# Optimization experiments

Measured on AMD Instinct MI355X. Metric: run time of the kernel, lower is better.

Reference implementation:

```python
import jax, jax.numpy as jnp
import numpy as np

EPS = 1e-5

def setup_inputs() -> dict:
    key = jax.random.key(0)
    kx, kq, kp = jax.random.split(key, 3)
    B, T, d = 4, 4096, 512
    x = jax.random.normal(kx, (B, T, d), dtype=jnp.float32)
    mask = jnp.tril(jnp.ones((T, T), dtype=jnp.int32))  # causal 0/1 mask
    gamma = jnp.ones((d,), dtype=jnp.float32)
    beta = jnp.zeros((d,), dtype=jnp.float32)
    Wqkv = jax.random.normal(kq, (d, 3 * d), dtype=jnp.float32) / np.sqrt(d)
    Wproj = jax.random.normal(kp, (d, d), dtype=jnp.float32) / np.sqrt(d)
    return {"x": x, "mask": mask, "gamma": gamma, "beta": beta, "Wqkv": Wqkv, "Wproj": Wproj}

def reference(x, mask, gamma, beta, Wqkv, Wproj):
    B, T, C = x.shape
    # LayerNorm over last dim
    mu = jnp.mean(x, axis=-1, keepdims=True)
    var = jnp.mean(jnp.square(x - mu), axis=-1, keepdims=True)
    xn = (x - mu) * jax.lax.rsqrt(var + EPS) * gamma + beta
    # QKV projection (no bias)
    qkv = xn @ Wqkv  # [B,T,3C]
    q, k, v = jnp.split(qkv, 3, axis=-1)
    scale = 1.0 / np.sqrt(C)
    dist = jnp.einsum('btc,bsc->bts', q, k) * scale  # [B,T,T]
    dist = jnp.where(mask[:T, :T] == 0, -jnp.inf, dist)
    attn = jax.nn.softmax(dist, axis=-1)
    out = jnp.einsum('bts,bsc->btc', attn, v)
    return out @ Wproj
```

## Files before the change

kernel.cpp:

```cpp
#include <hip/hip_runtime.h>

typedef short bf16x8 __attribute__((ext_vector_type(8)));
typedef float f32x4 __attribute__((ext_vector_type(4)));

#define AS1 __attribute__((address_space(1)))
#define AS3 __attribute__((address_space(3)))

__device__ __forceinline__ void async16(const void* g, void* l) {
    __builtin_amdgcn_global_load_lds((AS1 unsigned*)(unsigned long long)g,
                                     (AS3 unsigned*)l, 16, 0, 0);
}

__device__ __forceinline__ unsigned short f2bf(float f) {
    unsigned u = __builtin_bit_cast(unsigned, f);
    u += 0x7fffu + ((u >> 16) & 1u);
    return (unsigned short)(u >> 16);
}
__device__ __forceinline__ float bf2f(unsigned short s) {
    unsigned u = ((unsigned)s) << 16;
    return __builtin_bit_cast(float, u);
}

__global__ __launch_bounds__(256) void ln_bf16_kernel(
    const float* __restrict__ x, const float* __restrict__ gamma,
    const float* __restrict__ beta, unsigned short* __restrict__ xn, int nrows)
{
    int row = blockIdx.x * 4 + (threadIdx.x >> 6);
    int lane = threadIdx.x & 63;
    if (row >= nrows) return;
    const float4* xr = (const float4*)(x + (size_t)row * 512);
    float4 a = xr[lane], b = xr[lane + 64];
    float s = a.x + a.y + a.z + a.w + b.x + b.y + b.z + b.w;
    #pragma unroll
    for (int m = 1; m < 64; m <<= 1) s += __shfl_xor(s, m);
    float mu = s * (1.0f / 512.0f);
    float dx[8] = {a.x - mu, a.y - mu, a.z - mu, a.w - mu,
                   b.x - mu, b.y - mu, b.z - mu, b.w - mu};
    float ss = 0.f;
    #pragma unroll
    for (int i = 0; i < 8; ++i) ss += dx[i] * dx[i];
    #pragma unroll
    for (int m = 1; m < 64; m <<= 1) ss += __shfl_xor(ss, m);
    float rstd = rsqrtf(ss * (1.0f / 512.0f) + 1e-5f);
    const float4* gp = (const float4*)gamma;
    const float4* bp = (const float4*)beta;
    float4 g0 = gp[lane], g1 = gp[lane + 64], b0 = bp[lane], b1 = bp[lane + 64];
    float y[8];
    y[0] = dx[0] * rstd * g0.x + b0.x; y[1] = dx[1] * rstd * g0.y + b0.y;
    y[2] = dx[2] * rstd * g0.z + b0.z; y[3] = dx[3] * rstd * g0.w + b0.w;
    y[4] = dx[4] * rstd * g1.x + b1.x; y[5] = dx[5] * rstd * g1.y + b1.y;
    y[6] = dx[6] * rstd * g1.z + b1.z; y[7] = dx[7] * rstd * g1.w + b1.w;
    ushort4* orow = (ushort4*)(xn + (size_t)row * 512);
    orow[lane]      = make_ushort4(f2bf(y[0]), f2bf(y[1]), f2bf(y[2]), f2bf(y[3]));
    orow[lane + 64] = make_ushort4(f2bf(y[4]), f2bf(y[5]), f2bf(y[6]), f2bf(y[7]));
}

__global__ __launch_bounds__(256) void transpose_w(
    const float* __restrict__ in, unsigned short* __restrict__ outT, int R, int Cd)
{
    __shared__ float tile[64][65];
    int r0 = blockIdx.x * 64, c0 = blockIdx.y * 64;
    int lr = threadIdx.x >> 6, lc = threadIdx.x & 63;
    #pragma unroll
    for (int i = 0; i < 16; ++i) {
        int r = i * 4 + lr;
        tile[r][lc] = in[(size_t)(r0 + r) * Cd + c0 + lc];
    }
    __syncthreads();
    #pragma unroll
    for (int i = 0; i < 16; ++i) {
        int r = i * 4 + lr;
        outT[(size_t)(c0 + r) * R + r0 + lc] = f2bf(tile[lc][r]);
    }
}

__global__ __launch_bounds__(256) void gemm_qkv(
    const unsigned short* __restrict__ A, const unsigned short* __restrict__ Bt,
    unsigned short* __restrict__ qkOut, unsigned short* __restrict__ vtp)
{
    __shared__ unsigned short As[128 * 64];
    __shared__ unsigned short Bs[128 * 64];
    const int tid = threadIdx.x;
    const int w = tid >> 6, lane = tid & 63, quad = lane >> 4, l15 = lane & 15;
    const int wm = w >> 1, wn = w & 1;
    const size_t m0 = (size_t)blockIdx.x * 128, n0 = (size_t)blockIdx.y * 128;
    f32x4 zero = {0.f, 0.f, 0.f, 0.f};
    f32x4 acc[4][4];
    #pragma unroll
    for (int i = 0; i < 4; ++i)
        #pragma unroll
        for (int j = 0; j < 4; ++j) acc[i][j] = zero;

    for (int k0 = 0; k0 < 512; k0 += 64) {
        __syncthreads();
        #pragma unroll
        for (int r = 0; r < 4; ++r) {
            int s = r * 256 + w * 64 + lane;
            int row = s >> 3, x = s & 7, g = x ^ (row & 7);
            async16(A + (m0 + row) * 512 + k0 + g * 8,
                    (char*)As + (size_t)(r * 256 + w * 64) * 16);
        }
        #pragma unroll
        for (int r = 0; r < 4; ++r) {
            int s = r * 256 + w * 64 + lane;
            int row = s >> 3, x = s & 7, g = x ^ (row & 7);
            async16(Bt + (n0 + row) * 512 + k0 + g * 8,
                    (char*)Bs + (size_t)(r * 256 + w * 64) * 16);
        }
        __syncthreads();
        #pragma unroll
        for (int ks = 0; ks < 2; ++ks) {
            bf16x8 af[4], bf[4];
            int cc = ks * 4 + quad;
            #pragma unroll
            for (int mt = 0; mt < 4; ++mt) {
                int row = wm * 64 + mt * 16 + l15;
                int x = cc ^ (row & 7);
                af[mt] = *(const bf16x8*)(As + row * 64 + x * 8);
            }
            #pragma unroll
            for (int nt = 0; nt < 4; ++nt) {
                int row = wn * 64 + nt * 16 + l15;
                int x = cc ^ (row & 7);
                bf[nt] = *(const bf16x8*)(Bs + row * 64 + x * 8);
            }
            #pragma unroll
            for (int mt = 0; mt < 4; ++mt)
                #pragma unroll
                for (int nt = 0; nt < 4; ++nt)
                    acc[mt][nt] = __builtin_amdgcn_mfma_f32_16x16x32_bf16(
                        af[mt], bf[nt], acc[mt][nt], 0, 0, 0);
        }
    }
    if (n0 < 1024) {
        #pragma unroll
        for (int mt = 0; mt < 4; ++mt)
            #pragma unroll
            for (int nt = 0; nt < 4; ++nt)
                #pragma unroll
                for (int r = 0; r < 4; ++r) {
                    size_t grow = m0 + wm * 64 + mt * 16 + quad * 4 + r;
                    size_t gcol = n0 + wn * 64 + nt * 16 + l15;
                    qkOut[grow * 1024 + gcol] = f2bf(acc[mt][nt][r]);
                }
    } else {
        const int b = (int)(m0 >> 12);
        const int tb = (int)(m0 & 4095);
        #pragma unroll
        for (int mt = 0; mt < 4; ++mt)
            #pragma unroll
            for (int nt = 0; nt < 4; ++nt)
                #pragma unroll
                for (int r = 0; r < 4; ++r) {
                    int t = tb + wm * 64 + mt * 16 + quad * 4 + r;
                    int vcol = (int)(n0 - 1024) + wn * 64 + nt * 16 + l15;
                    int jt = t >> 5;
                    int x = (t >> 3) & 3;
                    int slot = vcol * 4 + ((x ^ (vcol >> 1)) & 3);
                    vtp[(size_t)(b * 128 + jt) * 16384 + slot * 8 + (t & 7)] =
                        f2bf(acc[mt][nt][r]);
                }
    }
}

__global__ __launch_bounds__(256) void gemm_bt(
    const unsigned short* __restrict__ A, const unsigned short* __restrict__ Bt,
    void* __restrict__ Cp, int M, int N, int K, int lda, int ldb, int ldc, int outBf16)
{
    __shared__ unsigned short As[128 * 64];
    __shared__ unsigned short Bs[128 * 64];
    const int tid = threadIdx.x;
    const int w = tid >> 6, lane = tid & 63, quad = lane >> 4, l15 = lane & 15;
    const int wm = w >> 1, wn = w & 1;
    const size_t m0 = (size_t)blockIdx.x * 128, n0 = (size_t)blockIdx.y * 128;
    f32x4 zero = {0.f, 0.f, 0.f, 0.f};
    f32x4 acc[4][4];
    #pragma unroll
    for (int i = 0; i < 4; ++i)
        #pragma unroll
        for (int j = 0; j < 4; ++j) acc[i][j] = zero;

    for (int k0 = 0; k0 < K; k0 += 64) {
        __syncthreads();
        #pragma unroll
        for (int r = 0; r < 4; ++r) {
            int s = r * 256 + w * 64 + lane;
            int row = s >> 3, x = s & 7, g = x ^ (row & 7);
            async16(A + (m0 + row) * lda + k0 + g * 8,
                    (char*)As + (size_t)(r * 256 + w * 64) * 16);
        }
        #pragma unroll
        for (int r = 0; r < 4; ++r) {
            int s = r * 256 + w * 64 + lane;
            int row = s >> 3, x = s & 7, g = x ^ (row & 7);
            async16(Bt + (n0 + row) * ldb + k0 + g * 8,
                    (char*)Bs + (size_t)(r * 256 + w * 64) * 16);
        }
        __syncthreads();
        #pragma unroll
        for (int ks = 0; ks < 2; ++ks) {
            bf16x8 af[4], bf[4];
            int cc = ks * 4 + quad;
            #pragma unroll
            for (int mt = 0; mt < 4; ++mt) {
                int row = wm * 64 + mt * 16 + l15;
                int x = cc ^ (row & 7);
                af[mt] = *(const bf16x8*)(As + row * 64 + x * 8);
            }
            #pragma unroll
            for (int nt = 0; nt < 4; ++nt) {
                int row = wn * 64 + nt * 16 + l15;
                int x = cc ^ (row & 7);
                bf[nt] = *(const bf16x8*)(Bs + row * 64 + x * 8);
            }
            #pragma unroll
            for (int mt = 0; mt < 4; ++mt)
                #pragma unroll
                for (int nt = 0; nt < 4; ++nt)
                    acc[mt][nt] = __builtin_amdgcn_mfma_f32_16x16x32_bf16(
                        af[mt], bf[nt], acc[mt][nt], 0, 0, 0);
        }
    }
    #pragma unroll
    for (int mt = 0; mt < 4; ++mt)
        #pragma unroll
        for (int nt = 0; nt < 4; ++nt)
            #pragma unroll
            for (int r = 0; r < 4; ++r) {
                size_t grow = m0 + wm * 64 + mt * 16 + quad * 4 + r;
                size_t gcol = n0 + wn * 64 + nt * 16 + l15;
                float v = acc[mt][nt][r];
                if (outBf16) ((unsigned short*)Cp)[grow * ldc + gcol] = f2bf(v);
                else         ((float*)Cp)[grow * ldc + gcol] = v;
            }
}

__global__ __launch_bounds__(256, 2) void attn_kernel(
    const unsigned short* __restrict__ qk,
    const unsigned short* __restrict__ vtp,
    unsigned short* __restrict__ ph0, unsigned short* __restrict__ ph1,
    float* __restrict__ lp)
{
    __shared__ unsigned short Ks[32 * 512];
    __shared__ unsigned short Vs[32 * 512];
    __shared__ unsigned short Ps[64 * 40];

    const int id = blockIdx.x;
    const int cu = id & 255, hi = id >> 8;
    const int b = cu & 3;
    const int q = hi ? (63 - (cu >> 2)) : (cu >> 2);
    const int h = hi;

    const int jt0 = h ? (q + 1) : 0;
    const int jtN = h ? (2 * q + 2) : (q + 1);

    const int tid = threadIdx.x, w = tid >> 6, lane = tid & 63;
    const int quad = lane >> 4, l15 = lane & 15;
    const float scale = 0.04419417382415922f;
    f32x4 zero = {0.f, 0.f, 0.f, 0.f};

    const unsigned short* kbase = qk + (size_t)(b * 4096) * 1024 + 512;
    const unsigned short* vbase = vtp + (size_t)(b * 128) * 16384;
    unsigned short* dst = h ? ph1 : ph0;

    const int gE = (lane & ~7) | ((lane ^ w) & 7);
    const int gO = (lane & ~7) | ((lane ^ (w + 4)) & 7);
    const size_t kOffE = (size_t)w * 1024 + (size_t)gE * 8;
    const size_t kOffO = (size_t)(w + 4) * 1024 + (size_t)gO * 8;
    const size_t vOff  = (size_t)tid * 8;

    bf16x8 qf[16];
    {
        const unsigned short* qb =
            qk + (size_t)(b * 4096 + q * 64 + w * 16 + l15) * 1024;
        #pragma unroll
        for (int ks = 0; ks < 16; ++ks)
            qf[ks] = *(const bf16x8*)(qb + ks * 32 + quad * 8);
    }
    f32x4 o[4][8];
    #pragma unroll
    for (int i = 0; i < 4; ++i)
        #pragma unroll
        for (int d = 0; d < 8; ++d) o[i][d] = zero;
    float li[4] = {0.f, 0.f, 0.f, 0.f};

    for (int jt = jt0; jt < jtN; ++jt) {
        __syncthreads();
        {
            const unsigned short* kg = kbase + (size_t)jt * 32768;
            #pragma unroll
            for (int rr = 0; rr < 4; ++rr) {
                async16(kg + (size_t)(2 * rr) * 4096 + kOffE,
                        (char*)Ks + (size_t)((2 * rr) * 256 + w * 64) * 16);
                async16(kg + (size_t)(2 * rr) * 4096 + kOffO,
                        (char*)Ks + (size_t)((2 * rr + 1) * 256 + w * 64) * 16);
            }
            const unsigned short* vg = vbase + (size_t)jt * 16384 + vOff;
            #pragma unroll
            for (int rnd = 0; rnd < 8; ++rnd)
                async16(vg + (size_t)rnd * 2048,
                        (char*)Vs + (size_t)(rnd * 256 + w * 64) * 16);
        }
        __syncthreads();

        f32x4 sa[2];
        sa[0] = zero; sa[1] = zero;
        __builtin_amdgcn_s_setprio(1);
        #pragma unroll
        for (int ks = 0; ks < 16; ++ks) {
            int cc = ks * 4 + quad;
            #pragma unroll
            for (int nt = 0; nt < 2; ++nt) {
                int jr = nt * 16 + l15;
                int xg = (cc & ~7) | ((cc ^ jr) & 7);
                bf16x8 kf = *(const bf16x8*)(Ks + jr * 512 + xg * 8);
                sa[nt] = __builtin_amdgcn_mfma_f32_16x16x32_bf16(
                    qf[ks], kf, sa[nt], 0, 0, 0);
            }
        }
        __builtin_amdgcn_s_setprio(0);
        const int trow = q * 64 + w * 16 + quad * 4;
        #pragma unroll
        for (int r = 0; r < 4; ++r) {
            #pragma unroll
            for (int nt = 0; nt < 2; ++nt) {
                int col = jt * 32 + nt * 16 + l15;
                float sv = sa[nt][r] * scale;
                float pv = __expf(fminf(sv, 60.f));
                if (col > trow + r) pv = 0.f;
                li[r] += pv;
                Ps[(w * 16 + quad * 4 + r) * 40 + nt * 16 + l15] = f2bf(pv);
            }
        }
        asm volatile("s_waitcnt lgkmcnt(0)" ::: "memory");
        __builtin_amdgcn_s_barrier();

        __builtin_amdgcn_s_setprio(1);
        #pragma unroll
        for (int ph = 0; ph < 2; ++ph) {
            bf16x8 vfr[4];
            #pragma unroll
            for (int d4 = 0; d4 < 4; ++d4) {
                int cch = (w * 8 + ph * 4 + d4) * 16 + l15;
                int slot = cch * 4 + ((quad ^ (cch >> 1)) & 3);
                vfr[d4] = *(const bf16x8*)(Vs + slot * 8);
            }
            #pragma unroll
            for (int qi = 0; qi < 4; ++qi) {
                bf16x8 pa = *(const bf16x8*)(Ps + (qi * 16 + l15) * 40 + quad * 8);
                #pragma unroll
                for (int d4 = 0; d4 < 4; ++d4)
                    o[qi][ph * 4 + d4] = __builtin_amdgcn_mfma_f32_16x16x32_bf16(
                        pa, vfr[d4], o[qi][ph * 4 + d4], 0, 0, 0);
            }
        }
        __builtin_amdgcn_s_setprio(0);
    }

    #pragma unroll
    for (int r = 0; r < 4; ++r) {
        float s = li[r];
        s += __shfl_xor(s, 1);
        s += __shfl_xor(s, 2);
        s += __shfl_xor(s, 4);
        s += __shfl_xor(s, 8);
        if (l15 == 0)
            lp[h * 16384 + b * 4096 + q * 64 + w * 16 + quad * 4 + r] = s;
    }
    unsigned short* ob = dst + (size_t)(b * 4096 + q * 64) * 512 + w * 128;
    #pragma unroll
    for (int qi = 0; qi < 4; ++qi)
        #pragma unroll
        for (int df = 0; df < 8; ++df)
            #pragma unroll
            for (int r = 0; r < 4; ++r)
                ob[(size_t)(qi * 16 + quad * 4 + r) * 512 + df * 16 + l15] =
                    f2bf(o[qi][df][r]);
}

__global__ __launch_bounds__(256) void combine_kernel(
    const unsigned short* __restrict__ ph0, const unsigned short* __restrict__ ph1,
    const float* __restrict__ lp, unsigned short* __restrict__ att)
{
    int t = blockIdx.x * 4 + (threadIdx.x >> 6);
    int lane = threadIdx.x & 63;
    float inv = 1.0f / (lp[t] + lp[16384 + t]);
    const ushort4* pa = (const ushort4*)(ph0 + (size_t)t * 512 + lane * 8);
    const ushort4* pb = (const ushort4*)(ph1 + (size_t)t * 512 + lane * 8);
    ushort4* po = (ushort4*)(att + (size_t)t * 512 + lane * 8);
    #pragma unroll
    for (int i = 0; i < 2; ++i) {
        ushort4 a = pa[i], b = pb[i];
        po[i] = make_ushort4(
            f2bf((bf2f(a.x) + bf2f(b.x)) * inv),
            f2bf((bf2f(a.y) + bf2f(b.y)) * inv),
            f2bf((bf2f(a.z) + bf2f(b.z)) * inv),
            f2bf((bf2f(a.w) + bf2f(b.w)) * inv));
    }
}

extern "C" void kernel_launch(void* const* d_in, const int* in_sizes, int n_in,
                              void* d_out, int out_size, void* d_ws, size_t ws_size,
                              hipStream_t stream)
{
    const float* x     = (const float*)d_in[0];
    const float* gamma = (const float*)d_in[2];
    const float* beta  = (const float*)d_in[3];
    const float* Wqkv  = (const float*)d_in[4];
    const float* Wproj = (const float*)d_in[5];
    float* out = (float*)d_out;

    char* ws = (char*)d_ws;
    unsigned short* qk     = (unsigned short*)(ws);
    unsigned short* ph1    = (unsigned short*)(ws + 33554432);
    unsigned short* vtp    = (unsigned short*)(ws + 50331648);
    unsigned short* xn     = (unsigned short*)(ws + 67108864);
    unsigned short* wqkvT  = (unsigned short*)(ws + 83886080);
    unsigned short* wprojT = (unsigned short*)(ws + 85458944);
    unsigned short* ph0    = xn;
    float*          lp     = (float*)wqkvT;
    unsigned short* att    = vtp;

    ln_bf16_kernel<<<4096, 256, 0, stream>>>(x, gamma, beta, xn, 16384);
    transpose_w<<<dim3(8, 24), 256, 0, stream>>>(Wqkv, wqkvT, 512, 1536);
    transpose_w<<<dim3(8, 8), 256, 0, stream>>>(Wproj, wprojT, 512, 512);
    gemm_qkv<<<dim3(128, 12), 256, 0, stream>>>(xn, wqkvT, qk, vtp);
    attn_kernel<<<512, 256, 0, stream>>>(qk, vtp, ph0, ph1, lp);
    combine_kernel<<<4096, 256, 0, stream>>>(ph0, ph1, lp, att);
    gemm_bt<<<dim3(128, 4), 256, 0, stream>>>(att, wprojT, out,
                                              16384, 512, 512, 512, 512, 512, 0);
}
```

Before: 351.0 us.

## Double-buffer K tiles in LDS and read V fragments directly from global

The attention loop now double-buffers K tiles in shared memory, prefetching the next K tile asynchronously while the current tile is computed. V is no longer staged through LDS. Each wave loads its V fragments straight from global memory into registers, and the V-transpose writer drops its XOR swizzle to match the new unswizzled layout. This aims to hide K load latency and cut LDS traffic and capacity per block, at the cost of exposed global-load latency on V inside the loop and more registers.

New measurement: 350.9 us. About the same (-0.0%).

```diff
diff --git a/kernel.cpp b/kernel.cpp
--- a/kernel.cpp
+++ b/kernel.cpp
@@ -156,8 +156,8 @@
                     int vcol = (int)(n0 - 1024) + wn * 64 + nt * 16 + l15;
                     int jt = t >> 5;
                     int x = (t >> 3) & 3;
-                    int slot = vcol * 4 + ((x ^ (vcol >> 1)) & 3);
-                    vtp[(size_t)(b * 128 + jt) * 16384 + slot * 8 + (t & 7)] =
+                    vtp[(size_t)(b * 128 + jt) * 16384
+                        + (size_t)(vcol * 4 + x) * 8 + (t & 7)] =
                         f2bf(acc[mt][nt][r]);
                 }
     }
@@ -241,8 +241,7 @@
     unsigned short* __restrict__ ph0, unsigned short* __restrict__ ph1,
     float* __restrict__ lp)
 {
-    __shared__ unsigned short Ks[32 * 512];
-    __shared__ unsigned short Vs[32 * 512];
+    __shared__ unsigned short Ks[2][32 * 512];
     __shared__ unsigned short Ps[64 * 40];
 
     const int id = blockIdx.x;
@@ -267,7 +266,7 @@
     const int gO = (lane & ~7) | ((lane ^ (w + 4)) & 7);
     const size_t kOffE = (size_t)w * 1024 + (size_t)gE * 8;
     const size_t kOffO = (size_t)(w + 4) * 1024 + (size_t)gO * 8;
-    const size_t vOff  = (size_t)tid * 8;
+    const size_t vLane = (size_t)w * 4096 + (size_t)l15 * 32 + (size_t)quad * 8;
 
     bf16x8 qf[16];
     {
@@ -284,24 +283,24 @@
         for (int d = 0; d < 8; ++d) o[i][d] = zero;
     float li[4] = {0.f, 0.f, 0.f, 0.f};
 
+    #define STAGE_K(BUF, T)                                                      \
+    {                                                                            \
+        const unsigned short* kg = kbase + (size_t)(T) * 32768;                  \
+        _Pragma("unroll")                                                        \
+        for (int rr = 0; rr < 4; ++rr) {                                         \
+            async16(kg + (size_t)(2 * rr) * 4096 + kOffE,                        \
+                    (char*)(&Ks[BUF][0]) + (size_t)((2 * rr) * 256 + w * 64) * 16);\
+            async16(kg + (size_t)(2 * rr) * 4096 + kOffO,                        \
+                    (char*)(&Ks[BUF][0]) + (size_t)((2 * rr + 1) * 256 + w * 64) * 16);\
+        }                                                                        \
+    }
+
+    STAGE_K(0, jt0);
+    __syncthreads();
+    int cur = 0;
+
     for (int jt = jt0; jt < jtN; ++jt) {
-        __syncthreads();
-        {
-            const unsigned short* kg = kbase + (size_t)jt * 32768;
-            #pragma unroll
-            for (int rr = 0; rr < 4; ++rr) {
-                async16(kg + (size_t)(2 * rr) * 4096 + kOffE,
-                        (char*)Ks + (size_t)((2 * rr) * 256 + w * 64) * 16);
-                async16(kg + (size_t)(2 * rr) * 4096 + kOffO,
-                        (char*)Ks + (size_t)((2 * rr + 1) * 256 + w * 64) * 16);
-            }
-            const unsigned short* vg = vbase + (size_t)jt * 16384 + vOff;
-            #pragma unroll
-            for (int rnd = 0; rnd < 8; ++rnd)
-                async16(vg + (size_t)rnd * 2048,
-                        (char*)Vs + (size_t)(rnd * 256 + w * 64) * 16);
-        }
-        __syncthreads();
+        if (jt + 1 < jtN) STAGE_K(cur ^ 1, jt + 1);
 
         f32x4 sa[2];
         sa[0] = zero; sa[1] = zero;
@@ -313,7 +312,7 @@
             for (int nt = 0; nt < 2; ++nt) {
                 int jr = nt * 16 + l15;
                 int xg = (cc & ~7) | ((cc ^ jr) & 7);
-                bf16x8 kf = *(const bf16x8*)(Ks + jr * 512 + xg * 8);
+                bf16x8 kf = *(const bf16x8*)(&Ks[cur][jr * 512 + xg * 8]);
                 sa[nt] = __builtin_amdgcn_mfma_f32_16x16x32_bf16(
                     qf[ks], kf, sa[nt], 0, 0, 0);
             }
@@ -335,27 +334,25 @@
         asm volatile("s_waitcnt lgkmcnt(0)" ::: "memory");
         __builtin_amdgcn_s_barrier();
 
+        const unsigned short* vt = vbase + (size_t)jt * 16384 + vLane;
+        bf16x8 vfr[8];
+        #pragma unroll
+        for (int i = 0; i < 8; ++i)
+            vfr[i] = *(const bf16x8*)(vt + (size_t)i * 512);
         __builtin_amdgcn_s_setprio(1);
         #pragma unroll
-        for (int ph = 0; ph < 2; ++ph) {
-            bf16x8 vfr[4];
-            #pragma unroll
-            for (int d4 = 0; d4 < 4; ++d4) {
-                int cch = (w * 8 + ph * 4 + d4) * 16 + l15;
-                int slot = cch * 4 + ((quad ^ (cch >> 1)) & 3);
-                vfr[d4] = *(const bf16x8*)(Vs + slot * 8);
-            }
-            #pragma unroll
-            for (int qi = 0; qi < 4; ++qi) {
-                bf16x8 pa = *(const bf16x8*)(Ps + (qi * 16 + l15) * 40 + quad * 8);
-                #pragma unroll
-                for (int d4 = 0; d4 < 4; ++d4)
-                    o[qi][ph * 4 + d4] = __builtin_amdgcn_mfma_f32_16x16x32_bf16(
-                        pa, vfr[d4], o[qi][ph * 4 + d4], 0, 0, 0);
-            }
+        for (int qi = 0; qi < 4; ++qi) {
+            bf16x8 pa = *(const bf16x8*)(Ps + (qi * 16 + l15) * 40 + quad * 8);
+            #pragma unroll
+            for (int i = 0; i < 8; ++i)
+                o[qi][i] = __builtin_amdgcn_mfma_f32_16x16x32_bf16(
+                    pa, vfr[i], o[qi][i], 0, 0, 0);
         }
         __builtin_amdgcn_s_setprio(0);
-    }
+        __syncthreads();
+        cur ^= 1;
+    }
+    #undef STAGE_K
 
     #pragma unroll
     for (int r = 0; r < 4; ++r) {
```
